# Kernel tuning notes

Measured on AMD Instinct MI355X. Metric: run time of the kernel, lower is better.

## Reference

```python
import jax, jax.numpy as jnp
import numpy as np


def _layernorm(x, g, b, eps=1e-5):
    m = jnp.mean(x, axis=-1, keepdims=True)
    v = jnp.var(x, axis=-1, keepdims=True)
    return (x - m) / jnp.sqrt(v + eps) * g + b


def _gat_layer(x, W, a1, a2, Wo, bo, diag_mask):
    # x: [B,N,D]; W: [H,D,D]; a1,a2: [H,D]; Wo: [H*D,D]; bo: [D]
    # Additive-attention split: a.[h_i;h_j] = a1.h_i + a2.h_j (same math as
    # the torch concat+linear, since the score layer is linear and bias-free).
    h = jnp.einsum('bni,hio->bhno', x, W)                       # [B,H,N,D]
    s1 = jnp.einsum('bhnd,hd->bhn', h, a1)                      # [B,H,N]
    s2 = jnp.einsum('bhnd,hd->bhn', h, a2)                      # [B,H,N]
    e = jax.nn.leaky_relu(s1[..., :, None] + s2[..., None, :], 0.2)  # [B,H,N,N]
    # fully-connected adjacency = ones - eye -> mask only the diagonal
    e = jnp.where(diag_mask, -jnp.inf, e)
    alpha = jax.nn.softmax(e, axis=-1)                          # [B,H,N,N]
    out = jnp.einsum('bhij,bhjd->bhid', alpha, h)               # [B,H,N,D]
    B, H, N, D = out.shape
    out = out.transpose(0, 2, 1, 3).reshape(B, N, H * D)        # concat heads
    return out @ Wo + bo                                        # [B,N,D]


def setup_inputs() -> dict:
    key = jax.random.key(0)
    ks = jax.random.split(key, 9)
    B, N, IN, D, H, L = 16, 1024, 7, 128, 4, 3
    s = 0.1
    return {
        'node_features': jax.random.normal(ks[0], (B, N, IN), jnp.float32),
        'Wp': jax.random.normal(ks[1], (IN, D), jnp.float32) * s,
        'bp': jax.random.normal(ks[2], (D,), jnp.float32) * s,
        'W':  jax.random.normal(ks[3], (L, H, D, D), jnp.float32) * s,
        'a1': jax.random.normal(ks[4], (L, H, D), jnp.float32) * s,
        'a2': jax.random.normal(ks[5], (L, H, D), jnp.float32) * s,
        'Wo': jax.random.normal(ks[6], (L, H * D, D), jnp.float32) * s,
        'bo': jax.random.normal(ks[7], (L, D), jnp.float32) * s,
        'gamma': jnp.ones((L, D), jnp.float32),
        'beta': jnp.zeros((L, D), jnp.float32),
    }


def reference(node_features, Wp, bp, W, a1, a2, Wo, bo, gamma, beta):
    B, N, _ = node_features.shape
    L = W.shape[0]
    diag_mask = jnp.eye(N, dtype=bool)  # adjacency==0 positions of (ones-eye)
    x = node_features @ Wp + bp         # input_proj
    for i in range(L):
        x_new = _gat_layer(x, W[i], a1[i], a2[i], Wo[i], bo[i], diag_mask)
        if i > 0:
            x = _layernorm(x + x_new, gamma[i], beta[i])  # residual + LN
        else:
            x = _layernorm(x_new, gamma[i], beta[i])
        if i < L - 1:
            x = jax.nn.relu(x)
    return x
```

## Files before the change

kernel.cpp:

```cpp
#include <hip/hip_runtime.h>
#include <hip/hip_bf16.h>

typedef __attribute__((ext_vector_type(8))) _Float16 f16x8;
typedef __attribute__((ext_vector_type(2))) _Float16 f16x2;
typedef __attribute__((ext_vector_type(8))) short short8;
typedef __attribute__((ext_vector_type(4))) short short4v;
typedef __attribute__((ext_vector_type(4))) float f32x4;

typedef const __attribute__((address_space(1))) unsigned int* gas_ptr;
typedef __attribute__((address_space(3))) unsigned int* las_ptr;
#define GLDS16(gp, lp) \
  __builtin_amdgcn_global_load_lds((gas_ptr)(gp), (las_ptr)(lp), 16, 0, 0)

#if __has_builtin(__builtin_amdgcn_fdot2)
#define FDOT2(a, b, c) __builtin_amdgcn_fdot2((a), (b), (c), false)
#else
__device__ __forceinline__ float FDOT2(f16x2 a, f16x2 b, float c) {
  return c + (float)a[0] * (float)b[0] + (float)a[1] * (float)b[1];
}
#endif

union h8u {
  f16x8 v;
  f16x2 h[4];
};

__device__ __forceinline__ short f2h(float f) {
  union { _Float16 h; short s; } u; u.h = (_Float16)f; return u.s;
}
__device__ __forceinline__ float h2f(short s) {
  union { short s; _Float16 h; } u; u.s = s; return (float)u.h;
}

__global__ __launch_bounds__(256) void k_init(const float* __restrict__ W,
                                              const float* __restrict__ Wo,
                                              const float* __restrict__ nf,
                                              const float* __restrict__ Wp,
                                              const float* __restrict__ bp,
                                              short* __restrict__ WT,
                                              short* __restrict__ WoT,
                                              short* __restrict__ xh) {
  if (blockIdx.x < 1536) {
    int idx = blockIdx.x * 256 + threadIdx.x;
    if (idx < 3 * 512 * 128) {
      int l = idx >> 16, rem = idx & 65535;
      int c = rem >> 7, k = rem & 127;
      int h = c >> 7, o = c & 127;
      WT[idx] = f2h(W[(((l * 4 + h) * 128 + k) << 7) + o]);
    } else {
      int j = idx - 3 * 512 * 128;
      int l = j >> 16, rem = j & 65535;
      int d = rem >> 9, c = rem & 511;
      WoT[j] = f2h(Wo[((l * 512 + c) << 7) + d]);
    }
  } else {
    int idx = (blockIdx.x - 1536) * 256 + threadIdx.x;
    int bn = idx >> 7, d = idx & 127;
    float acc = bp[d];
    const float* nr = nf + bn * 7;
#pragma unroll
    for (int i = 0; i < 7; ++i) acc += nr[i] * Wp[(i << 7) + d];
    xh[idx] = f2h(acc);
  }
}

__global__ __launch_bounds__(256) void k_gemm_h(const short* __restrict__ xh,
                                                const short* __restrict__ WT,
                                                short* __restrict__ hT,
                                                const float* __restrict__ a1,
                                                const float* __restrict__ a2,
                                                float* __restrict__ s1g,
                                                float* __restrict__ s2g) {
  __shared__ __align__(16) short As[128 * 64];
  __shared__ __align__(16) short Bs[128 * 64];
  __shared__ float sred[2][2][128];
  const int t = threadIdx.x;
  const int bn0 = blockIdx.x << 7;
  const int head = blockIdx.y;
  const int c0 = head << 7;
  const int w = t >> 6, lane = t & 63, lr = lane & 15, lq = lane >> 4;
  const int wr = w >> 1, wc = w & 1;
  const int grow = (w << 5) + (lane >> 3);
  const int gcol = ((lane & 7) ^ (lane >> 3)) << 3;
  const short* gsrcA = xh + ((bn0 + grow) << 7) + gcol;
  const short* gsrcB = WT + ((c0 + grow) << 7) + gcol;
  f32x4 acc[4][4] = {};
  for (int k0 = 0; k0 < 128; k0 += 64) {
    {
      short* ldsbA = &As[(w << 5) << 6];
      short* ldsbB = &Bs[(w << 5) << 6];
#pragma unroll
      for (int i_ = 0; i_ < 4; ++i_) {
        GLDS16(gsrcA + ((i_ << 3) << 7) + k0, ldsbA + ((i_ << 3) << 6));
        GLDS16(gsrcB + ((i_ << 3) << 7) + k0, ldsbB + ((i_ << 3) << 6));
      }
    }
    __syncthreads();
#pragma unroll
    for (int kk = 0; kk < 2; ++kk) {
      f16x8 a[4], b[4];
#pragma unroll
      for (int m = 0; m < 4; ++m) {
        const int r_ = wr * 64 + m * 16 + lr;
        const int slot_ = ((kk << 2) + lq) ^ (r_ & 7);
        a[m] = *(const f16x8*)(&As[(r_ << 6) + (slot_ << 3)]);
      }
#pragma unroll
      for (int n = 0; n < 4; ++n) {
        const int r_ = wc * 64 + n * 16 + lr;
        const int slot_ = ((kk << 2) + lq) ^ (r_ & 7);
        b[n] = *(const f16x8*)(&Bs[(r_ << 6) + (slot_ << 3)]);
      }
#pragma unroll
      for (int m = 0; m < 4; ++m)
#pragma unroll
        for (int n = 0; n < 4; ++n)
          acc[m][n] = __builtin_amdgcn_mfma_f32_16x16x32_f16(a[m], b[n], acc[m][n], 0, 0, 0);
    }
    __syncthreads();
  }
  const int b = bn0 >> 10;
  const int nb = bn0 & 1023;
  float a1v[4], a2v[4];
#pragma unroll
  for (int n = 0; n < 4; ++n) {
    int d = wc * 64 + n * 16 + lr;
    a1v[n] = a1[(head << 7) + d];
    a2v[n] = a2[(head << 7) + d];
  }
#pragma unroll
  for (int m = 0; m < 4; ++m)
#pragma unroll
    for (int r = 0; r < 4; ++r) {
      float v1 = 0.f, v2 = 0.f;
#pragma unroll
      for (int n = 0; n < 4; ++n) {
        v1 += acc[m][n][r] * a1v[n];
        v2 += acc[m][n][r] * a2v[n];
      }
#pragma unroll
      for (int off = 1; off < 16; off <<= 1) {
        v1 += __shfl_xor(v1, off);
        v2 += __shfl_xor(v2, off);
      }
      if (lr == 0) {
        int row = wr * 64 + m * 16 + (lq << 2) + r;
        sred[wc][0][row] = v1;
        sred[wc][1][row] = v2;
      }
    }
#pragma unroll
  for (int m = 0; m < 4; ++m) {
    int nrow = nb + wr * 64 + m * 16 + (lq << 2);
#pragma unroll
    for (int n = 0; n < 4; ++n) {
      int d = wc * 64 + n * 16 + lr;
      long base = ((long)((((b << 2) + head) << 7) + d) << 10) + nrow;
      short4v v;
      v[0] = f2h(acc[m][n][0]); v[1] = f2h(acc[m][n][1]);
      v[2] = f2h(acc[m][n][2]); v[3] = f2h(acc[m][n][3]);
      *(short4v*)(hT + base) = v;
    }
  }
  __syncthreads();
  {
    const int bh_ = (b << 2) + head;
    if (t < 128)
      s1g[(bh_ << 10) + nb + t] = sred[0][0][t] + sred[1][0][t];
    else
      s2g[(bh_ << 10) + nb + (t - 128)] = sred[0][1][t - 128] + sred[1][1][t - 128];
  }
}

__global__ __launch_bounds__(256) void k_attn(const short* __restrict__ hT,
                                              const float* __restrict__ s1,
                                              const float* __restrict__ s2g,
                                              short* __restrict__ attn) {
  __shared__ __align__(16) short Hs[3][128 * 64];
  __shared__ __align__(16) _Float16 Esh[1024];
  __shared__ __align__(16) _Float16 Fsh[1024];
  __shared__ float red[4];
  const int bh = blockIdx.x, it = blockIdx.y;
  const int i0 = it << 7;
  const int t = threadIdx.x;
  const int w = t >> 6, lane = t & 63, lr = lane & 15, lq = lane >> 4;

  const short* hTb = hT + ((long)bh << 17);
  const int grow = (w << 5) + (lane >> 3);
  const int gcol = ((lane & 7) ^ (lane >> 3)) << 3;
  const short* gsrc = hTb + ((long)grow << 10) + gcol;

#define STAGE(buf, J0)                                             \
  do {                                                             \
    short* ldsb = &Hs[buf][(w << 5) << 6];                         \
    _Pragma("unroll") for (int i_ = 0; i_ < 4; ++i_)               \
        GLDS16(gsrc + ((long)(i_ << 3) << 10) + (J0),              \
               ldsb + ((i_ << 3) << 6));                           \
  } while (0)

  STAGE(0, 0);
  STAGE(1, 64);

  f32x4 v2 = *(const f32x4*)&s2g[(bh << 10) + (t << 2)];
  {
    float mx = fmaxf(fmaxf(v2[0], v2[1]), fmaxf(v2[2], v2[3]));
#pragma unroll
    for (int off = 1; off < 64; off <<= 1) mx = fmaxf(mx, __shfl_xor(mx, off));
    if ((t & 63) == 0) red[t >> 6] = mx;
  }
  __syncthreads();
  const float smax = fmaxf(fmaxf(red[0], red[1]), fmaxf(red[2], red[3]));
  {
    short4v e, f;
#pragma unroll
    for (int q = 0; q < 4; ++q) {
      e[q] = f2h(__expf(v2[q] - smax));
      f[q] = f2h(__expf(0.2f * (v2[q] - smax)));
    }
    *(short4v*)&Esh[t << 2] = e;
    *(short4v*)&Fsh[t << 2] = f;
  }

  f16x8 Ai8[2], Bi8[2];
  const f16x2 one2 = {(_Float16)1.f, (_Float16)1.f};
  f16x8 dmask[2];
  float dsum[2] = {0.f, 0.f};
#pragma unroll
  for (int m = 0; m < 2; ++m) {
    const int rblk = (w << 5) + (m << 4) + lr;
    float s1v = s1[(bh << 10) + i0 + rblk];
    float x = s1v + smax;
    float mi = fmaxf(x, 0.2f * x);
    _Float16 A_ = (_Float16)__expf(x - mi);
    _Float16 B_ = (_Float16)__expf(0.2f * x - mi);
#pragma unroll
    for (int e = 0; e < 8; ++e) { Ai8[m][e] = A_; Bi8[m][e] = B_; }
    const int lqz = ((m << 1) + (lr >> 3)) & 3, ez = lr & 7;
#pragma unroll
    for (int e = 0; e < 8; ++e)
      dmask[m][e] = (lq == lqz && e == ez) ? (_Float16)0.f : (_Float16)1.f;
  }
  const int jtd = (it << 1) + (w >> 1);
  const int kkd = w & 1;
  f32x4 acc[2][8] = {};
  __syncthreads();

#define TILE(buf, jt, DIAG)                                                    \
  do {                                                                         \
    _Pragma("unroll") for (int kk = 0; kk < 2; ++kk) {                         \
      const int ebase = ((jt) << 6) + (kk << 5) + (lq << 3);                   \
      f16x8 ev8 = *(const f16x8*)&Esh[ebase];                                  \
      f16x8 fv8 = *(const f16x8*)&Fsh[ebase];                                  \
      f16x8 bf[8];                                                             \
      _Pragma("unroll") for (int n = 0; n < 8; ++n) {                          \
        const int r_ = (n << 4) + lr;                                          \
        const int slot_ = ((kk << 2) + lq) ^ (r_ & 7);                         \
        bf[n] = *(const f16x8*)(&Hs[buf][(r_ << 6) + (slot_ << 3)]);           \
      }                                                                        \
      f16x8 af[2];                                                             \
      _Pragma("unroll") for (int m = 0; m < 2; ++m) {                          \
        f16x8 pm = __builtin_elementwise_max(Ai8[m] * ev8, Bi8[m] * fv8);      \
        if ((DIAG) && kk == kkd) pm = pm * dmask[m];                           \
        af[m] = pm;                                                            \
        h8u u_; u_.v = pm;                                                     \
        _Pragma("unroll") for (int p = 0; p < 4; ++p)                          \
            dsum[m] = FDOT2(u_.h[p], one2, dsum[m]);                           \
      }                                                                        \
      _Pragma("unroll") for (int m = 0; m < 2; ++m)                            \
        _Pragma("unroll") for (int n = 0; n < 8; ++n)                          \
            acc[m][n] = __builtin_amdgcn_mfma_f32_16x16x32_f16(                \
                af[m], bf[n], acc[m][n], 0, 0, 0);                             \
    }                                                                          \
  } while (0)

  int cur = 0;
#pragma unroll 1
  for (int jt = 0; jt < 16; ++jt) {
    if (jt < 15) {
      asm volatile("s_waitcnt vmcnt(4)" ::: "memory");
    } else {
      asm volatile("s_waitcnt vmcnt(0)" ::: "memory");
    }
    __builtin_amdgcn_s_barrier();
    if (jt < 14) STAGE((cur == 0 ? 2 : cur - 1), (jt + 2) << 6);
    TILE(cur, jt, jt == jtd);
    cur = (cur == 2) ? 0 : cur + 1;
  }

  const int b = bh >> 2, head = bh & 3;
#pragma unroll
  for (int m = 0; m < 2; ++m) {
    float s = dsum[m];
    s += __shfl_xor(s, 16);
    s += __shfl_xor(s, 32);
    float rs = 1.f / s;
    f32x4 d4;
#pragma unroll
    for (int q = 0; q < 4; ++q)
      d4[q] = __shfl(rs, (lane & 48) | ((lq << 2) + q));
    int irow = i0 + (w << 5) + (m << 4) + (lq << 2);
#pragma unroll
    for (int n = 0; n < 8; ++n) {
      int d = (n << 4) + lr;
      long base = ((long)((b << 10) + irow) << 9) + (head << 7) + d;
      attn[base] = f2h(acc[m][n][0] * d4[0]);
      attn[base + 512] = f2h(acc[m][n][1] * d4[1]);
      attn[base + 1024] = f2h(acc[m][n][2] * d4[2]);
      attn[base + 1536] = f2h(acc[m][n][3] * d4[3]);
    }
  }
#undef STAGE
#undef TILE
}

template <int HAS_RES, int DO_RELU, int WRITE_OUT>
__global__ __launch_bounds__(256) void k_outproj(const short* __restrict__ attn,
                                                 const short* __restrict__ WoT,
                                                 const float* __restrict__ bo,
                                                 const float* __restrict__ gamma,
                                                 const float* __restrict__ beta,
                                                 short* __restrict__ xh,
                                                 float* __restrict__ outp) {
  __shared__ __align__(16) short As[32 * 64];
  __shared__ __align__(16) short Bs[128 * 64];
  __shared__ float sredS[2][32], sredQ[2][32];
  const int t = threadIdx.x;
  const int bn0 = blockIdx.x << 5;
  const int w = t >> 6, lane = t & 63, lr = lane & 15, lq = lane >> 4;
  const int wm = w & 1, wn = w >> 1;
  f32x4 acc[4] = {};
  const int gcol = ((lane & 7) ^ (lane >> 3)) << 3;
  const int growA = (w << 3) + (lane >> 3);
  const short* gsrcA = attn + ((long)(bn0 + growA) << 9) + gcol;
  const int growB = (w << 5) + (lane >> 3);
  const short* gsrcB = WoT + (growB << 9) + gcol;
  for (int k0 = 0; k0 < 512; k0 += 64) {
    {
      GLDS16(gsrcA + k0, &As[(w << 3) << 6]);
      short* ldsbB = &Bs[(w << 5) << 6];
#pragma unroll
      for (int i_ = 0; i_ < 4; ++i_)
        GLDS16(gsrcB + ((i_ << 3) << 9) + k0, ldsbB + ((i_ << 3) << 6));
    }
    __syncthreads();
#pragma unroll
    for (int kk = 0; kk < 2; ++kk) {
      const int rA = (wm << 4) + lr;
      const int slotA = ((kk << 2) + lq) ^ (rA & 7);
      f16x8 a = *(const f16x8*)(&As[(rA << 6) + (slotA << 3)]);
#pragma unroll
      for (int nn = 0; nn < 4; ++nn) {
        const int r_ = (wn << 6) + (nn << 4) + lr;
        const int slot_ = ((kk << 2) + lq) ^ (r_ & 7);
        f16x8 b = *(const f16x8*)(&Bs[(r_ << 6) + (slot_ << 3)]);
        acc[nn] = __builtin_amdgcn_mfma_f32_16x16x32_f16(a, b, acc[nn], 0, 0, 0);
      }
    }
    __syncthreads();
  }
  float v[4][4], gam[4], bet[4];
#pragma unroll
  for (int nn = 0; nn < 4; ++nn) {
    int d = (wn << 6) + (nn << 4) + lr;
    float bv = bo[d];
    gam[nn] = gamma[d];
    bet[nn] = beta[d];
#pragma unroll
    for (int r = 0; r < 4; ++r) {
      float x = acc[nn][r] + bv;
      if (HAS_RES) x += h2f(xh[((bn0 + (wm << 4) + (lq << 2) + r) << 7) + d]);
      v[nn][r] = x;
    }
  }
#pragma unroll
  for (int r = 0; r < 4; ++r) {
    float s = 0.f, q = 0.f;
#pragma unroll
    for (int nn = 0; nn < 4; ++nn) { s += v[nn][r]; q += v[nn][r] * v[nn][r]; }
#pragma unroll
    for (int mk = 1; mk < 16; mk <<= 1) { s += __shfl_xor(s, mk); q += __shfl_xor(q, mk); }
    if (lr == 0) {
      int row = (wm << 4) + (lq << 2) + r;
      sredS[wn][row] = s;
      sredQ[wn][row] = q;
    }
  }
  __syncthreads();
#pragma unroll
  for (int r = 0; r < 4; ++r) {
    int rloc = (wm << 4) + (lq << 2) + r;
    float S = sredS[0][rloc] + sredS[1][rloc];
    float Q = sredQ[0][rloc] + sredQ[1][rloc];
    float mean = S * 0.0078125f;
    float var = Q * 0.0078125f - mean * mean;
    float rstd = rsqrtf(var + 1e-5f);
    int row = bn0 + rloc;
#pragma unroll
    for (int nn = 0; nn < 4; ++nn) {
      int d = (wn << 6) + (nn << 4) + lr;
      float o = (v[nn][r] - mean) * rstd * gam[nn] + bet[nn];
      if (DO_RELU) o = fmaxf(o, 0.f);
      if (WRITE_OUT) outp[(row << 7) + d] = o;
      else xh[(row << 7) + d] = f2h(o);
    }
  }
}

extern "C" void kernel_launch(void* const* d_in, const int* in_sizes, int n_in,
                              void* d_out, int out_size, void* d_ws, size_t ws_size,
                              hipStream_t stream) {
  const float* nf = (const float*)d_in[0];
  const float* Wp = (const float*)d_in[1];
  const float* bp = (const float*)d_in[2];
  const float* W = (const float*)d_in[3];
  const float* a1 = (const float*)d_in[4];
  const float* a2 = (const float*)d_in[5];
  const float* Wo = (const float*)d_in[6];
  const float* bo = (const float*)d_in[7];
  const float* gamma = (const float*)d_in[8];
  const float* beta = (const float*)d_in[9];
  float* outp = (float*)d_out;

  char* ws = (char*)d_ws;
  short* xh = (short*)(ws);
  short* hT = (short*)(ws + (4ll << 20));
  short* attn = (short*)(ws + (20ll << 20));
  float* s1 = (float*)(ws + (36ll << 20));
  float* s2g = (float*)(ws + (36ll << 20) + (256ll << 10));
  short* WT = (short*)(ws + (37ll << 20));
  short* WoT = (short*)(ws + (37ll << 20) + 393216);

  k_init<<<9728, 256, 0, stream>>>(W, Wo, nf, Wp, bp, WT, WoT, xh);
  for (int l = 0; l < 3; ++l) {
    k_gemm_h<<<dim3(128, 4), 256, 0, stream>>>(xh, WT + l * 65536, hT,
                                               a1 + l * 512, a2 + l * 512, s1, s2g);
    k_attn<<<dim3(64, 8), 256, 0, stream>>>(hT, s1, s2g, attn);
    if (l == 0)
      k_outproj<0, 1, 0><<<512, 256, 0, stream>>>(attn, WoT + l * 65536, bo + l * 128,
                                                  gamma + l * 128, beta + l * 128, xh, outp);
    else if (l == 1)
      k_outproj<1, 1, 0><<<512, 256, 0, stream>>>(attn, WoT + l * 65536, bo + l * 128,
                                                  gamma + l * 128, beta + l * 128, xh, outp);
    else
      k_outproj<1, 0, 1><<<512, 256, 0, stream>>>(attn, WoT + l * 65536, bo + l * 128,
                                                  gamma + l * 128, beta + l * 128, xh, outp);
  }
}
```

Measured before the change: 143.5 us.

## Prefetch both K tiles in gemm_h and triple-buffer outproj K loop

In k_gemm_h, both 64-wide K tiles are now issued up front into two separate LDS buffers. Each tile is waited on with a partial vmcnt, so compute on the first tile can start while the second is still loading. In k_outproj, the 8-step K loop becomes a 3-stage ring buffer that prefetches two tiles ahead, with partial waits and a single barrier per step instead of two syncthreads. This aims to hide global-to-LDS latency, at the cost of more LDS per block, which may reduce occupancy. It also relies on hand-set vmcnt counts matching the number of loads issued.

Result: no change. 143.1 us, median of 2 (-0.3%).

```diff
diff --git a/kernel.cpp b/kernel.cpp
--- a/kernel.cpp
+++ b/kernel.cpp
@@ -71,8 +71,8 @@
                                                 const float* __restrict__ a2,
                                                 float* __restrict__ s1g,
                                                 float* __restrict__ s2g) {
-  __shared__ __align__(16) short As[128 * 64];
-  __shared__ __align__(16) short Bs[128 * 64];
+  __shared__ __align__(16) short As[2][128 * 64];
+  __shared__ __align__(16) short Bs[2][128 * 64];
   __shared__ float sred[2][2][128];
   const int t = threadIdx.x;
   const int bn0 = blockIdx.x << 7;
@@ -85,17 +85,23 @@
   const short* gsrcA = xh + ((bn0 + grow) << 7) + gcol;
   const short* gsrcB = WT + ((c0 + grow) << 7) + gcol;
   f32x4 acc[4][4] = {};
-  for (int k0 = 0; k0 < 128; k0 += 64) {
-    {
-      short* ldsbA = &As[(w << 5) << 6];
-      short* ldsbB = &Bs[(w << 5) << 6];
-#pragma unroll
-      for (int i_ = 0; i_ < 4; ++i_) {
-        GLDS16(gsrcA + ((i_ << 3) << 7) + k0, ldsbA + ((i_ << 3) << 6));
-        GLDS16(gsrcB + ((i_ << 3) << 7) + k0, ldsbB + ((i_ << 3) << 6));
-      }
-    }
-    __syncthreads();
+#pragma unroll
+  for (int kb = 0; kb < 2; ++kb) {
+    short* ldsbA = &As[kb][(w << 5) << 6];
+    short* ldsbB = &Bs[kb][(w << 5) << 6];
+#pragma unroll
+    for (int i_ = 0; i_ < 4; ++i_) {
+      GLDS16(gsrcA + ((i_ << 3) << 7) + (kb << 6), ldsbA + ((i_ << 3) << 6));
+      GLDS16(gsrcB + ((i_ << 3) << 7) + (kb << 6), ldsbB + ((i_ << 3) << 6));
+    }
+  }
+#pragma unroll 1
+  for (int kb = 0; kb < 2; ++kb) {
+    if (kb == 0)
+      asm volatile("s_waitcnt vmcnt(8)" ::: "memory");
+    else
+      asm volatile("s_waitcnt vmcnt(0)" ::: "memory");
+    __builtin_amdgcn_s_barrier();
 #pragma unroll
     for (int kk = 0; kk < 2; ++kk) {
       f16x8 a[4], b[4];
@@ -103,13 +109,13 @@
       for (int m = 0; m < 4; ++m) {
         const int r_ = wr * 64 + m * 16 + lr;
         const int slot_ = ((kk << 2) + lq) ^ (r_ & 7);
-        a[m] = *(const f16x8*)(&As[(r_ << 6) + (slot_ << 3)]);
+        a[m] = *(const f16x8*)(&As[kb][(r_ << 6) + (slot_ << 3)]);
       }
 #pragma unroll
       for (int n = 0; n < 4; ++n) {
         const int r_ = wc * 64 + n * 16 + lr;
         const int slot_ = ((kk << 2) + lq) ^ (r_ & 7);
-        b[n] = *(const f16x8*)(&Bs[(r_ << 6) + (slot_ << 3)]);
+        b[n] = *(const f16x8*)(&Bs[kb][(r_ << 6) + (slot_ << 3)]);
       }
 #pragma unroll
       for (int m = 0; m < 4; ++m)
@@ -117,7 +123,6 @@
         for (int n = 0; n < 4; ++n)
           acc[m][n] = __builtin_amdgcn_mfma_f32_16x16x32_f16(a[m], b[n], acc[m][n], 0, 0, 0);
     }
-    __syncthreads();
   }
   const int b = bn0 >> 10;
   const int nb = bn0 & 1023;
@@ -321,8 +326,8 @@
                                                  const float* __restrict__ beta,
                                                  short* __restrict__ xh,
                                                  float* __restrict__ outp) {
-  __shared__ __align__(16) short As[32 * 64];
-  __shared__ __align__(16) short Bs[128 * 64];
+  __shared__ __align__(16) short As3[3][32 * 64];
+  __shared__ __align__(16) short Bs3[3][128 * 64];
   __shared__ float sredS[2][32], sredQ[2][32];
   const int t = threadIdx.x;
   const int bn0 = blockIdx.x << 5;
@@ -334,30 +339,44 @@
   const short* gsrcA = attn + ((long)(bn0 + growA) << 9) + gcol;
   const int growB = (w << 5) + (lane >> 3);
   const short* gsrcB = WoT + (growB << 9) + gcol;
-  for (int k0 = 0; k0 < 512; k0 += 64) {
-    {
-      GLDS16(gsrcA + k0, &As[(w << 3) << 6]);
-      short* ldsbB = &Bs[(w << 5) << 6];
-#pragma unroll
-      for (int i_ = 0; i_ < 4; ++i_)
-        GLDS16(gsrcB + ((i_ << 3) << 9) + k0, ldsbB + ((i_ << 3) << 6));
-    }
-    __syncthreads();
+
+#define OSTAGE(buf, K0)                                            \
+  do {                                                             \
+    GLDS16(gsrcA + (K0), &As3[buf][(w << 3) << 6]);                \
+    short* ldsbB = &Bs3[buf][(w << 5) << 6];                       \
+    _Pragma("unroll") for (int i_ = 0; i_ < 4; ++i_)               \
+        GLDS16(gsrcB + ((i_ << 3) << 9) + (K0),                    \
+               ldsbB + ((i_ << 3) << 6));                          \
+  } while (0)
+
+  OSTAGE(0, 0);
+  OSTAGE(1, 64);
+  int cur = 0;
+#pragma unroll 1
+  for (int jt = 0; jt < 8; ++jt) {
+    if (jt < 7) {
+      asm volatile("s_waitcnt vmcnt(5)" ::: "memory");
+    } else {
+      asm volatile("s_waitcnt vmcnt(0)" ::: "memory");
+    }
+    __builtin_amdgcn_s_barrier();
+    if (jt < 6) OSTAGE((cur == 0 ? 2 : cur - 1), (jt + 2) << 6);
 #pragma unroll
     for (int kk = 0; kk < 2; ++kk) {
       const int rA = (wm << 4) + lr;
       const int slotA = ((kk << 2) + lq) ^ (rA & 7);
-      f16x8 a = *(const f16x8*)(&As[(rA << 6) + (slotA << 3)]);
+      f16x8 a = *(const f16x8*)(&As3[cur][(rA << 6) + (slotA << 3)]);
 #pragma unroll
       for (int nn = 0; nn < 4; ++nn) {
         const int r_ = (wn << 6) + (nn << 4) + lr;
         const int slot_ = ((kk << 2) + lq) ^ (r_ & 7);
-        f16x8 b = *(const f16x8*)(&Bs[(r_ << 6) + (slot_ << 3)]);
+        f16x8 b = *(const f16x8*)(&Bs3[cur][(r_ << 6) + (slot_ << 3)]);
         acc[nn] = __builtin_amdgcn_mfma_f32_16x16x32_f16(a, b, acc[nn], 0, 0, 0);
       }
     }
-    __syncthreads();
-  }
+    cur = (cur == 2) ? 0 : cur + 1;
+  }
+#undef OSTAGE
   float v[4][4], gam[4], bet[4];
 #pragma unroll
   for (int nn = 0; nn < 4; ++nn) {
```
